# Performance work log

Hardware: AMD Instinct MI355X
Metric: run time of the kernel (lower is better)

Reference implementation:

```python
import jax, jax.numpy as jnp
import numpy as np

TRACE_LR = 0.1
TRACE_DECAY = 0.99
ERASE_LR = 1.0
EPS = 1e-8


def setup_inputs() -> dict:
    key = jax.random.key(0)
    k1, k2, k3, k4 = jax.random.split(key, 4)
    B, H, S, D = 8, 8, 4096, 64
    DM = 768
    Q = jax.random.normal(k1, (B, H, S, D), dtype=jnp.float32)
    V = jax.random.normal(k2, (B, H, S, D), dtype=jnp.float32)
    # value_traces buffer (small random state so erase path is non-trivial)
    trace = jax.random.normal(k3, (H, D, D), dtype=jnp.float32) * 0.01
    # W_out: Linear(H*D -> DM), weight shape (DM, H*D), out = x @ W.T
    W_out = jax.random.normal(k4, (DM, H * D), dtype=jnp.float32) / np.sqrt(H * D)
    return {"Q": Q, "V": V, "trace": trace, "W_out": W_out}


def _hebbian_write(Q, V, trace):
    """Erase-before-write + decayed Hebbian outer-product update.

    Q, V: (B, H, S, D); trace: (H, D, D). Shift-1 offset: key at i, value at i+2.
    """
    B, H, S, D = Q.shape
    Q_store = Q[:, :, :-2, :]            # (B,H,S-2,D)
    V_store = V[:, :, 2:, :]             # (B,H,S-2,D)
    denom = B * (S - 2)
    # reconsolidation erasure of old associations along normalized keys
    Q_norm = jnp.clip(jnp.linalg.norm(Q_store, axis=-1, keepdims=True), EPS)
    Q_erase = Q_store / Q_norm
    V_old = jnp.einsum('bhip,hpq->bhiq', Q_erase, trace)
    erase = jnp.einsum('bhip,bhiq->hpq', Q_erase, V_old) / denom
    trace = trace - ERASE_LR * erase
    # Hebbian outer-product write
    update = jnp.einsum('bhip,bhiq->hpq', Q_store, V_store) / denom
    return TRACE_DECAY * trace + TRACE_LR * update


def reference(Q, V, trace, W_out):
    B, H, S, D = Q.shape
    new_trace = _hebbian_write(Q, V, trace)
    # shift-1 retrieval: Q_addr at position i uses Q from position i-1
    Q_addr = jnp.concatenate(
        [jnp.zeros_like(Q[:, :, :1, :]), Q[:, :, :-1, :]], axis=2)  # (B,H,S,D)
    V_ret = jnp.einsum('bhsp,hpq->bhsq', Q_addr, new_trace)          # (B,H,S,D)
    V_ret = V_ret.transpose(0, 2, 1, 3).reshape(B, S, H * D)         # (B,S,H*D)
    return V_ret @ W_out.T                                           # (B,S,d_model)
```

## Files before the change

kernel.cpp:

```cpp
#include <hip/hip_runtime.h>

#define B_ 8
#define H_ 8
#define S_ 4096
#define D_ 64
#define DM_ 768
#define NSTORE 4094
#define DENOM 32752.0f

typedef short bfrag_t __attribute__((ext_vector_type(8)));
typedef float f32x4_t __attribute__((ext_vector_type(4)));
typedef unsigned short us8_t __attribute__((ext_vector_type(8)));

__device__ inline unsigned short f2bf(float x) {
    unsigned int u = __float_as_uint(x);
    unsigned int r = (u + 0x7fffu + ((u >> 16) & 1u)) >> 16;
    return (unsigned short)r;
}

__global__ __launch_bounds__(256, 2) void gram_kernel(
    const float* __restrict__ Q, const float* __restrict__ V,
    float* __restrict__ gG, float* __restrict__ gU,
    unsigned short* __restrict__ Qbf, int writeQbf) {
    const int split = blockIdx.x, h = blockIdx.y, b = blockIdx.z;
    const int t = threadIdx.x;
    const int wave = t >> 6, lane = t & 63;
    const int quad = lane >> 4, l15 = lane & 15;
    __shared__ float Qs[64][68];
    __shared__ float Vs[64][68];
    __shared__ float scale[64];
    __shared__ __align__(16) unsigned short QT[64][72];
    __shared__ __align__(16) unsigned short QnT[64][72];
    __shared__ __align__(16) unsigned short VT[64][72];

    const size_t bh = (size_t)(b * H_ + h);
    const float* Qbh = Q + bh * S_ * D_;
    const float* Vbh = V + bh * S_ * D_;
    unsigned short* Qbfbh = Qbf + bh * S_ * D_;

    f32x4_t accG[4] = {}, accU[4] = {};
    const int r0 = split * 512;

    for (int tile = 0; tile < 8; ++tile) {
        const int rbase = r0 + tile * 64;
        #pragma unroll
        for (int i = 0; i < 4; ++i) {
            int f = i * 256 + t;
            int row = f >> 4, c4 = f & 15;
            int r = rbase + row;
            float4 q4 = *(const float4*)(Qbh + (size_t)r * D_ + c4 * 4);
            if (writeQbf) {
                ushort4 u;
                u.x = f2bf(q4.x); u.y = f2bf(q4.y); u.z = f2bf(q4.z); u.w = f2bf(q4.w);
                *(ushort4*)(Qbfbh + (size_t)r * D_ + c4 * 4) = u;
            }
            float4 v4 = make_float4(0.f, 0.f, 0.f, 0.f);
            if (r < NSTORE) {
                v4 = *(const float4*)(Vbh + (size_t)(r + 2) * D_ + c4 * 4);
            } else {
                q4 = make_float4(0.f, 0.f, 0.f, 0.f);
            }
            *(float4*)(&Qs[row][c4 * 4]) = q4;
            *(float4*)(&Vs[row][c4 * 4]) = v4;
            float ss = q4.x * q4.x + q4.y * q4.y + q4.z * q4.z + q4.w * q4.w;
            ss += __shfl_xor(ss, 1);
            ss += __shfl_xor(ss, 2);
            ss += __shfl_xor(ss, 4);
            ss += __shfl_xor(ss, 8);
            if ((t & 15) == 0) scale[row] = 1.0f / fmaxf(ss, 1e-16f);
        }
        __syncthreads();
        #pragma unroll
        for (int it = 0; it < 2; ++it) {
            int idx = it * 256 + t;
            int p = idx & 63, oct = idx >> 6;
            us8_t qt, qn, vt;
            #pragma unroll
            for (int j = 0; j < 8; ++j) {
                int r = oct * 8 + j;
                float s = scale[r];
                float q = Qs[r][p];
                float v = Vs[r][p];
                qt[j] = f2bf(q);
                qn[j] = f2bf(q * s);
                vt[j] = f2bf(v);
            }
            *(us8_t*)(&QT[p][oct * 8])  = qt;
            *(us8_t*)(&QnT[p][oct * 8]) = qn;
            *(us8_t*)(&VT[p][oct * 8])  = vt;
        }
        __syncthreads();
        #pragma unroll
        for (int c = 0; c < 2; ++c) {
            int k0 = c * 32 + quad * 8;
            bfrag_t ag = *(const bfrag_t*)(&QnT[wave * 16 + l15][k0]);
            bfrag_t au = *(const bfrag_t*)(&QT[wave * 16 + l15][k0]);
            #pragma unroll
            for (int j = 0; j < 4; ++j) {
                bfrag_t bq = *(const bfrag_t*)(&QT[j * 16 + l15][k0]);
                bfrag_t bv = *(const bfrag_t*)(&VT[j * 16 + l15][k0]);
                accG[j] = __builtin_amdgcn_mfma_f32_16x16x32_bf16(ag, bq, accG[j], 0, 0, 0);
                accU[j] = __builtin_amdgcn_mfma_f32_16x16x32_bf16(au, bv, accU[j], 0, 0, 0);
            }
        }
        __syncthreads();
    }
    float* gGh = gG + h * 4096;
    float* gUh = gU + h * 4096;
    #pragma unroll
    for (int j = 0; j < 4; ++j) {
        int col = j * 16 + l15;
        #pragma unroll
        for (int r = 0; r < 4; ++r) {
            int row = wave * 16 + quad * 4 + r;
            atomicAdd(&gGh[row * 64 + col], accG[j][r]);
            atomicAdd(&gUh[row * 64 + col], accU[j][r]);
        }
    }
}

__global__ __launch_bounds__(256) void trace_kernel(
    const float* __restrict__ gG, const float* __restrict__ gU,
    const float* __restrict__ trace, float* __restrict__ Tnew) {
    const int h = blockIdx.x, t = threadIdx.x;
    __shared__ float Gs[64][64];
    __shared__ float Ts[64][64];
    const float* Gh = gG + h * 4096;
    const float* Uh = gU + h * 4096;
    const float* Th = trace + h * 4096;
    float* To = Tnew + h * 4096;
    for (int k = 0; k < 16; ++k) {
        int e = k * 256 + t;
        Gs[e >> 6][e & 63] = Gh[e];
        Ts[e >> 6][e & 63] = Th[e];
    }
    __syncthreads();
    const float inv_denom = 1.0f / DENOM;
    for (int k = 0; k < 16; ++k) {
        int e = k * 256 + t;
        int p = e >> 6, q = e & 63;
        float dot = 0.f;
        #pragma unroll
        for (int r = 0; r < 64; ++r) dot += Gs[p][r] * Ts[r][q];
        To[e] = 0.99f * (Ts[p][q] - dot * inv_denom) + 0.1f * (Uh[e] * inv_denom);
    }
}

__global__ __launch_bounds__(256) void wc_kernel(
    const float* __restrict__ Tnew, const float* __restrict__ Wout,
    unsigned short* __restrict__ WcT) {
    const int nc = blockIdx.x, h = blockIdx.y, t = threadIdx.x;
    __shared__ float TsT[64][64];
    __shared__ float Ws[4][64];
    const float* Th = Tnew + h * 4096;
    for (int k = 0; k < 16; ++k) {
        int e = k * 256 + t;
        TsT[e & 63][e >> 6] = Th[e];
    }
    __syncthreads();
    const int p = t & 63, sub = t >> 6;
    for (int i = 0; i < 32; ++i) {
        int n = nc * 128 + i * 4 + sub;
        Ws[sub][p] = Wout[(size_t)n * 512 + h * 64 + p];
        __syncthreads();
        float acc = 0.f;
        #pragma unroll
        for (int q = 0; q < 64; ++q) acc += TsT[q][p] * Ws[sub][q];
        WcT[(size_t)n * 512 + h * 64 + p] = f2bf(acc);
        __syncthreads();
    }
}

template <bool QBF>
__global__ __launch_bounds__(256, 2) void matmul_kernel(
    const float* __restrict__ Qf, const unsigned short* __restrict__ Qb,
    const unsigned short* __restrict__ WcT, float* __restrict__ out) {
    const int mTile = blockIdx.x;
    const int nTile = blockIdx.y;
    const int t = threadIdx.x;
    const int wave = t >> 6, lane = t & 63;
    const int wm = wave >> 1, wn = wave & 1;
    const int quad = lane >> 4, l15 = lane & 15;
    __shared__ __align__(16) unsigned short As[128][72];
    __shared__ __align__(16) unsigned short Bs[128][72];
    const int b = mTile >> 5;
    const int s0 = (mTile & 31) * 128;
    const int nBase = nTile * 128;
    f32x4_t acc[4][4] = {};

    for (int h = 0; h < 8; ++h) {
        const size_t bh = (size_t)(b * H_ + h);
        if (QBF) {
            const unsigned short* Qbh = Qb + bh * S_ * D_;
            #pragma unroll
            for (int i = 0; i < 4; ++i) {
                int f = i * 256 + t;
                int row = f >> 3, c8 = f & 7;
                int s = s0 + row;
                uint4 u = make_uint4(0, 0, 0, 0);
                if (s > 0) u = *(const uint4*)(Qbh + (size_t)(s - 1) * D_ + c8 * 8);
                *(uint4*)(&As[row][c8 * 8]) = u;
            }
        } else {
            const float* Qbh = Qf + bh * S_ * D_;
            #pragma unroll
            for (int i = 0; i < 8; ++i) {
                int f = i * 256 + t;
                int row = f >> 4, c4 = f & 15;
                int s = s0 + row;
                float4 q4 = make_float4(0.f, 0.f, 0.f, 0.f);
                if (s > 0) q4 = *(const float4*)(Qbh + (size_t)(s - 1) * D_ + c4 * 4);
                ushort4 u;
                u.x = f2bf(q4.x); u.y = f2bf(q4.y); u.z = f2bf(q4.z); u.w = f2bf(q4.w);
                *(ushort4*)(&As[row][c4 * 4]) = u;
            }
        }
        #pragma unroll
        for (int i = 0; i < 4; ++i) {
            int f = i * 256 + t;
            int row = f >> 3, c8 = f & 7;
            uint4 w = *(const uint4*)(WcT + (size_t)(nBase + row) * 512 + h * 64 + c8 * 8);
            *(uint4*)(&Bs[row][c8 * 8]) = w;
        }
        __syncthreads();
        #pragma unroll
        for (int c = 0; c < 2; ++c) {
            int k0 = c * 32 + quad * 8;
            bfrag_t af[4], bf[4];
            #pragma unroll
            for (int i = 0; i < 4; ++i)
                af[i] = *(const bfrag_t*)(&As[wm * 64 + i * 16 + l15][k0]);
            #pragma unroll
            for (int j = 0; j < 4; ++j)
                bf[j] = *(const bfrag_t*)(&Bs[wn * 64 + j * 16 + l15][k0]);
            #pragma unroll
            for (int i = 0; i < 4; ++i)
                #pragma unroll
                for (int j = 0; j < 4; ++j)
                    acc[i][j] = __builtin_amdgcn_mfma_f32_16x16x32_bf16(af[i], bf[j], acc[i][j], 0, 0, 0);
        }
        __syncthreads();
    }
    const size_t mBase = (size_t)mTile * 128;
    #pragma unroll
    for (int i = 0; i < 4; ++i) {
        int mrow = wm * 64 + i * 16 + quad * 4;
        #pragma unroll
        for (int j = 0; j < 4; ++j) {
            int n = nBase + wn * 64 + j * 16 + l15;
            #pragma unroll
            for (int r = 0; r < 4; ++r)
                out[(mBase + mrow + r) * DM_ + n] = acc[i][j][r];
        }
    }
}

extern "C" void kernel_launch(void* const* d_in, const int* in_sizes, int n_in,
                              void* d_out, int out_size, void* d_ws, size_t ws_size,
                              hipStream_t stream) {
    const float* Q     = (const float*)d_in[0];
    const float* V     = (const float*)d_in[1];
    const float* trace = (const float*)d_in[2];
    const float* Wout  = (const float*)d_in[3];
    float* out = (float*)d_out;

    float* gG   = (float*)d_ws;
    float* gU   = gG + 32768;
    float* Tnew = gU + 32768;
    unsigned short* WcT = (unsigned short*)(Tnew + 32768);
    unsigned short* Qbf = WcT + 393216;

    const size_t qbf_bytes = (size_t)B_ * H_ * S_ * D_ * 2;
    const size_t base_bytes = 3u * 32768u * 4u + 393216u * 2u;
    const int useQbf = (ws_size >= base_bytes + qbf_bytes) ? 1 : 0;

    hipMemsetAsync(d_ws, 0, 2 * 32768 * sizeof(float), stream);
    gram_kernel<<<dim3(8, 8, 8), 256, 0, stream>>>(Q, V, gG, gU, Qbf, useQbf);
    trace_kernel<<<8, 256, 0, stream>>>(gG, gU, trace, Tnew);
    wc_kernel<<<dim3(6, 8), 256, 0, stream>>>(Tnew, Wout, WcT);
    if (useQbf)
        matmul_kernel<true><<<dim3(256, 6), 256, 0, stream>>>(Q, Qbf, WcT, out);
    else
        matmul_kernel<false><<<dim3(256, 6), 256, 0, stream>>>(Q, Qbf, WcT, out);
}
```

Baseline: 306.3 us.

## Rework gram, trace, wc and matmul kernels with async LDS copies and partial-sum reduction

The gram kernel now transposes and converts directly into XOR-swizzled bf16 LDS tiles without fp32 staging. When workspace allows, it uses twice as many splits and writes per-slab partials that a separate reduce kernel sums, replacing atomics and the memset. The trace and wc kernels are register-tiled with vector LDS reads. The bf16 matmul uses global_load_lds async 16-byte copies into swizzled LDS with three blocks per CU. This trades extra workspace and a partial-sum buffer round trip for less LDS staging, fewer bank conflicts and no atomics.

```diff
diff --git a/kernel.cpp b/kernel.cpp
--- a/kernel.cpp
+++ b/kernel.cpp
@@ -10,7 +10,6 @@
 
 typedef short bfrag_t __attribute__((ext_vector_type(8)));
 typedef float f32x4_t __attribute__((ext_vector_type(4)));
-typedef unsigned short us8_t __attribute__((ext_vector_type(8)));
 
 __device__ inline unsigned short f2bf(float x) {
     unsigned int u = __float_as_uint(x);
@@ -18,113 +17,136 @@
     return (unsigned short)r;
 }
 
-__global__ __launch_bounds__(256, 2) void gram_kernel(
+__device__ inline void async_copy16(const void* g, void* lds) {
+    __builtin_amdgcn_global_load_lds((__attribute__((address_space(1))) void*)g,
+                                     (__attribute__((address_space(3))) void*)lds,
+                                     16, 0, 0);
+}
+
+#define MFMA16(a, b, c) __builtin_amdgcn_mfma_f32_16x16x32_bf16((a), (b), (c), 0, 0, 0)
+
+template <bool PART>
+__global__ __launch_bounds__(256, 4) void gram_kernel(
     const float* __restrict__ Q, const float* __restrict__ V,
     float* __restrict__ gG, float* __restrict__ gU,
-    unsigned short* __restrict__ Qbf, int writeQbf) {
+    unsigned short* __restrict__ Qbf, float* __restrict__ gP, int writeQbf) {
     const int split = blockIdx.x, h = blockIdx.y, b = blockIdx.z;
+    const int nsplit = gridDim.x;
+    const int rowsPer = 4096 / nsplit;
+    const int nTiles = rowsPer >> 6;
     const int t = threadIdx.x;
     const int wave = t >> 6, lane = t & 63;
     const int quad = lane >> 4, l15 = lane & 15;
-    __shared__ float Qs[64][68];
-    __shared__ float Vs[64][68];
-    __shared__ float scale[64];
-    __shared__ __align__(16) unsigned short QT[64][72];
-    __shared__ __align__(16) unsigned short QnT[64][72];
-    __shared__ __align__(16) unsigned short VT[64][72];
+    __shared__ __align__(16) unsigned short QT[64 * 64];
+    __shared__ __align__(16) unsigned short QnT[64 * 64];
+    __shared__ __align__(16) unsigned short VT[64 * 64];
 
     const size_t bh = (size_t)(b * H_ + h);
     const float* Qbh = Q + bh * S_ * D_;
     const float* Vbh = V + bh * S_ * D_;
-    unsigned short* Qbfbh = Qbf + bh * S_ * D_;
+    unsigned short* Qo = Qbf + bh * S_ * D_;
 
     f32x4_t accG[4] = {}, accU[4] = {};
-    const int r0 = split * 512;
-
-    for (int tile = 0; tile < 8; ++tile) {
+    const int r0 = split * rowsPer;
+
+    for (int tile = 0; tile < nTiles; ++tile) {
         const int rbase = r0 + tile * 64;
         #pragma unroll
         for (int i = 0; i < 4; ++i) {
             int f = i * 256 + t;
-            int row = f >> 4, c4 = f & 15;
-            int r = rbase + row;
+            int rowl = f >> 4, c4 = f & 15;
+            int r = rbase + rowl;
             float4 q4 = *(const float4*)(Qbh + (size_t)r * D_ + c4 * 4);
             if (writeQbf) {
                 ushort4 u;
                 u.x = f2bf(q4.x); u.y = f2bf(q4.y); u.z = f2bf(q4.z); u.w = f2bf(q4.w);
-                *(ushort4*)(Qbfbh + (size_t)r * D_ + c4 * 4) = u;
+                *(ushort4*)(Qo + (size_t)r * D_ + c4 * 4) = u;
             }
             float4 v4 = make_float4(0.f, 0.f, 0.f, 0.f);
-            if (r < NSTORE) {
-                v4 = *(const float4*)(Vbh + (size_t)(r + 2) * D_ + c4 * 4);
-            } else {
-                q4 = make_float4(0.f, 0.f, 0.f, 0.f);
-            }
-            *(float4*)(&Qs[row][c4 * 4]) = q4;
-            *(float4*)(&Vs[row][c4 * 4]) = v4;
+            if (r < NSTORE) v4 = *(const float4*)(Vbh + (size_t)(r + 2) * D_ + c4 * 4);
+            else q4 = make_float4(0.f, 0.f, 0.f, 0.f);
             float ss = q4.x * q4.x + q4.y * q4.y + q4.z * q4.z + q4.w * q4.w;
             ss += __shfl_xor(ss, 1);
             ss += __shfl_xor(ss, 2);
             ss += __shfl_xor(ss, 4);
             ss += __shfl_xor(ss, 8);
-            if ((t & 15) == 0) scale[row] = 1.0f / fmaxf(ss, 1e-16f);
-        }
-        __syncthreads();
-        #pragma unroll
-        for (int it = 0; it < 2; ++it) {
-            int idx = it * 256 + t;
-            int p = idx & 63, oct = idx >> 6;
-            us8_t qt, qn, vt;
-            #pragma unroll
-            for (int j = 0; j < 8; ++j) {
-                int r = oct * 8 + j;
-                float s = scale[r];
-                float q = Qs[r][p];
-                float v = Vs[r][p];
-                qt[j] = f2bf(q);
-                qn[j] = f2bf(q * s);
-                vt[j] = f2bf(v);
-            }
-            *(us8_t*)(&QT[p][oct * 8])  = qt;
-            *(us8_t*)(&QnT[p][oct * 8]) = qn;
-            *(us8_t*)(&VT[p][oct * 8])  = vt;
+            float sc = 1.0f / fmaxf(ss, 1e-16f);
+            int col = rowl ^ ((c4 & 7) << 3);
+            float qa[4] = {q4.x, q4.y, q4.z, q4.w};
+            float va[4] = {v4.x, v4.y, v4.z, v4.w};
+            #pragma unroll
+            for (int j = 0; j < 4; ++j) {
+                int p = c4 * 4 + j;
+                QT [p * 64 + col] = f2bf(qa[j]);
+                QnT[p * 64 + col] = f2bf(qa[j] * sc);
+                VT [p * 64 + col] = f2bf(va[j]);
+            }
         }
         __syncthreads();
         #pragma unroll
         for (int c = 0; c < 2; ++c) {
-            int k0 = c * 32 + quad * 8;
-            bfrag_t ag = *(const bfrag_t*)(&QnT[wave * 16 + l15][k0]);
-            bfrag_t au = *(const bfrag_t*)(&QT[wave * 16 + l15][k0]);
+            int pA = wave * 16 + l15;
+            int offA = pA * 64 + (((c * 4 + quad) ^ ((pA >> 2) & 7)) << 3);
+            bfrag_t ag = *(const bfrag_t*)&QnT[offA];
+            bfrag_t au = *(const bfrag_t*)&QT[offA];
             #pragma unroll
             for (int j = 0; j < 4; ++j) {
-                bfrag_t bq = *(const bfrag_t*)(&QT[j * 16 + l15][k0]);
-                bfrag_t bv = *(const bfrag_t*)(&VT[j * 16 + l15][k0]);
-                accG[j] = __builtin_amdgcn_mfma_f32_16x16x32_bf16(ag, bq, accG[j], 0, 0, 0);
-                accU[j] = __builtin_amdgcn_mfma_f32_16x16x32_bf16(au, bv, accU[j], 0, 0, 0);
-            }
-        }
-        __syncthreads();
-    }
-    float* gGh = gG + h * 4096;
-    float* gUh = gU + h * 4096;
-    #pragma unroll
-    for (int j = 0; j < 4; ++j) {
-        int col = j * 16 + l15;
-        #pragma unroll
-        for (int r = 0; r < 4; ++r) {
-            int row = wave * 16 + quad * 4 + r;
-            atomicAdd(&gGh[row * 64 + col], accG[j][r]);
-            atomicAdd(&gUh[row * 64 + col], accU[j][r]);
-        }
-    }
+                int pB = j * 16 + l15;
+                int offB = pB * 64 + (((c * 4 + quad) ^ ((pB >> 2) & 7)) << 3);
+                bfrag_t bq = *(const bfrag_t*)&QT[offB];
+                bfrag_t bv = *(const bfrag_t*)&VT[offB];
+                accG[j] = MFMA16(ag, bq, accG[j]);
+                accU[j] = MFMA16(au, bv, accU[j]);
+            }
+        }
+        __syncthreads();
+    }
+    if (PART) {
+        const int slab = split * 8 + b;
+        float* base = gP + ((size_t)(h * 128 + slab) * 2) * 4096;
+        #pragma unroll
+        for (int j = 0; j < 4; ++j) {
+            int coln = j * 16 + l15;
+            #pragma unroll
+            for (int r = 0; r < 4; ++r) {
+                int row = wave * 16 + quad * 4 + r;
+                base[row * 64 + coln]        = accG[j][r];
+                base[4096 + row * 64 + coln] = accU[j][r];
+            }
+        }
+    } else {
+        float* gGh = gG + h * 4096;
+        float* gUh = gU + h * 4096;
+        #pragma unroll
+        for (int j = 0; j < 4; ++j) {
+            int coln = j * 16 + l15;
+            #pragma unroll
+            for (int r = 0; r < 4; ++r) {
+                int row = wave * 16 + quad * 4 + r;
+                atomicAdd(&gGh[row * 64 + coln], accG[j][r]);
+                atomicAdd(&gUh[row * 64 + coln], accU[j][r]);
+            }
+        }
+    }
+}
+
+__global__ __launch_bounds__(256) void reduce_kernel(
+    const float* __restrict__ gP, float* __restrict__ gG, float* __restrict__ gU) {
+    const int h = blockIdx.x, chunk = blockIdx.y, t = threadIdx.x;
+    const int arr = t >> 7, idx = chunk * 128 + (t & 127);
+    const float* base = gP + ((size_t)(h * 128) * 2 + arr) * 4096 + idx;
+    float s = 0.f;
+    #pragma unroll 8
+    for (int sl = 0; sl < 128; ++sl) s += base[(size_t)sl * 2 * 4096];
+    (arr ? gU : gG)[h * 4096 + idx] = s;
 }
 
 __global__ __launch_bounds__(256) void trace_kernel(
     const float* __restrict__ gG, const float* __restrict__ gU,
     const float* __restrict__ trace, float* __restrict__ Tnew) {
     const int h = blockIdx.x, t = threadIdx.x;
-    __shared__ float Gs[64][64];
-    __shared__ float Ts[64][64];
+    __shared__ float Gs[64][68];
+    __shared__ float Ts[64][68];
     const float* Gh = gG + h * 4096;
     const float* Uh = gU + h * 4096;
     const float* Th = trace + h * 4096;
@@ -135,14 +157,24 @@
         Ts[e >> 6][e & 63] = Th[e];
     }
     __syncthreads();
-    const float inv_denom = 1.0f / DENOM;
-    for (int k = 0; k < 16; ++k) {
-        int e = k * 256 + t;
-        int p = e >> 6, q = e & 63;
-        float dot = 0.f;
-        #pragma unroll
-        for (int r = 0; r < 64; ++r) dot += Gs[p][r] * Ts[r][q];
-        To[e] = 0.99f * (Ts[p][q] - dot * inv_denom) + 0.1f * (Uh[e] * inv_denom);
+    const int p = t >> 2, q0 = (t & 3) * 16;
+    f32x4_t acc[4] = {};
+    for (int r = 0; r < 64; ++r) {
+        float g = Gs[p][r];
+        #pragma unroll
+        for (int i = 0; i < 4; ++i) {
+            f32x4_t tv = *(const f32x4_t*)&Ts[r][q0 + i * 4];
+            acc[i] += g * tv;
+        }
+    }
+    const float inv = 1.0f / DENOM;
+    #pragma unroll
+    for (int i = 0; i < 4; ++i) {
+        int e = p * 64 + q0 + i * 4;
+        f32x4_t ts = *(const f32x4_t*)&Ts[p][q0 + i * 4];
+        f32x4_t uu = *(const f32x4_t*)(Uh + e);
+        f32x4_t res = 0.99f * (ts - acc[i] * inv) + (0.1f * inv) * uu;
+        *(f32x4_t*)(To + e) = res;
     }
 }
 
@@ -150,33 +182,122 @@
     const float* __restrict__ Tnew, const float* __restrict__ Wout,
     unsigned short* __restrict__ WcT) {
     const int nc = blockIdx.x, h = blockIdx.y, t = threadIdx.x;
-    __shared__ float TsT[64][64];
-    __shared__ float Ws[4][64];
+    __shared__ float TsT[64][68];
+    __shared__ float WbT[64][132];
     const float* Th = Tnew + h * 4096;
-    for (int k = 0; k < 16; ++k) {
-        int e = k * 256 + t;
-        TsT[e & 63][e >> 6] = Th[e];
+    #pragma unroll
+    for (int i = 0; i < 4; ++i) {
+        int f = i * 256 + t;
+        int p = f >> 4, q4 = f & 15;
+        float4 v = *(const float4*)(Th + p * 64 + q4 * 4);
+        TsT[q4 * 4 + 0][p] = v.x; TsT[q4 * 4 + 1][p] = v.y;
+        TsT[q4 * 4 + 2][p] = v.z; TsT[q4 * 4 + 3][p] = v.w;
+    }
+    #pragma unroll
+    for (int i = 0; i < 8; ++i) {
+        int f = i * 256 + t;
+        int n = f >> 4, q4 = f & 15;
+        float4 w = *(const float4*)(Wout + (size_t)(nc * 128 + n) * 512 + h * 64 + q4 * 4);
+        WbT[q4 * 4 + 0][n] = w.x; WbT[q4 * 4 + 1][n] = w.y;
+        WbT[q4 * 4 + 2][n] = w.z; WbT[q4 * 4 + 3][n] = w.w;
     }
     __syncthreads();
-    const int p = t & 63, sub = t >> 6;
-    for (int i = 0; i < 32; ++i) {
-        int n = nc * 128 + i * 4 + sub;
-        Ws[sub][p] = Wout[(size_t)n * 512 + h * 64 + p];
-        __syncthreads();
-        float acc = 0.f;
-        #pragma unroll
-        for (int q = 0; q < 64; ++q) acc += TsT[q][p] * Ws[sub][q];
-        WcT[(size_t)n * 512 + h * 64 + p] = f2bf(acc);
-        __syncthreads();
-    }
-}
-
-template <bool QBF>
-__global__ __launch_bounds__(256, 2) void matmul_kernel(
-    const float* __restrict__ Qf, const unsigned short* __restrict__ Qb,
-    const unsigned short* __restrict__ WcT, float* __restrict__ out) {
+    const int n0 = (t >> 4) * 8, p0 = (t & 15) * 4;
+    f32x4_t acc[8] = {};
+    for (int q = 0; q < 64; ++q) {
+        f32x4_t tp = *(const f32x4_t*)&TsT[q][p0];
+        f32x4_t w0 = *(const f32x4_t*)&WbT[q][n0];
+        f32x4_t w1 = *(const f32x4_t*)&WbT[q][n0 + 4];
+        #pragma unroll
+        for (int i = 0; i < 4; ++i) acc[i] += w0[i] * tp;
+        #pragma unroll
+        for (int i = 0; i < 4; ++i) acc[4 + i] += w1[i] * tp;
+    }
+    #pragma unroll
+    for (int i = 0; i < 8; ++i) {
+        int n = nc * 128 + n0 + i;
+        ushort4 u;
+        u.x = f2bf(acc[i][0]); u.y = f2bf(acc[i][1]);
+        u.z = f2bf(acc[i][2]); u.w = f2bf(acc[i][3]);
+        *(ushort4*)(WcT + (size_t)n * 512 + h * 64 + p0) = u;
+    }
+}
+
+__global__ __launch_bounds__(256, 3) void matmul_fast(
+    const unsigned short* __restrict__ Qb, const unsigned short* __restrict__ WcT,
+    float* __restrict__ out) {
     const int mTile = blockIdx.x;
     const int nTile = blockIdx.y;
+    const int t = threadIdx.x;
+    const int wave = t >> 6, lane = t & 63;
+    const int wm = wave >> 1, wn = wave & 1;
+    const int quad = lane >> 4, l15 = lane & 15;
+    __shared__ __align__(16) unsigned short As[128 * 64];
+    __shared__ __align__(16) unsigned short Bs[128 * 64];
+    const int b = mTile >> 5;
+    const int s0 = (mTile & 31) * 128;
+    const int nBase = nTile * 128;
+    const int rl8 = lane >> 3, g = lane & 7;
+    const int gs = g ^ rl8;
+    f32x4_t acc[4][4] = {};
+
+    for (int h = 0; h < 8; ++h) {
+        const unsigned short* Qbh = Qb + (size_t)(b * H_ + h) * S_ * D_;
+        #pragma unroll
+        for (int k = 0; k < 4; ++k) {
+            int ch = wave * 4 + k;
+            int row = ch * 8 + rl8;
+            int s = s0 + row;
+            int sc = (s > 0) ? (s - 1) : 0;
+            async_copy16(Qbh + (size_t)sc * 64 + gs * 8, &As[ch * 512 + lane * 8]);
+            async_copy16(WcT + (size_t)(nBase + row) * 512 + h * 64 + gs * 8,
+                         &Bs[ch * 512 + lane * 8]);
+        }
+        __syncthreads();
+        if (s0 == 0) {
+            if (t < 8) ((uint4*)As)[t] = make_uint4(0, 0, 0, 0);
+            __syncthreads();
+        }
+        #pragma unroll
+        for (int c = 0; c < 2; ++c) {
+            int gk = c * 4 + quad;
+            bfrag_t af[4], bf[4];
+            #pragma unroll
+            for (int i = 0; i < 4; ++i) {
+                int row = wm * 64 + i * 16 + l15;
+                af[i] = *(const bfrag_t*)&As[row * 64 + ((gk ^ (row & 7)) << 3)];
+            }
+            #pragma unroll
+            for (int j = 0; j < 4; ++j) {
+                int row = wn * 64 + j * 16 + l15;
+                bf[j] = *(const bfrag_t*)&Bs[row * 64 + ((gk ^ (row & 7)) << 3)];
+            }
+            #pragma unroll
+            for (int i = 0; i < 4; ++i)
+                #pragma unroll
+                for (int j = 0; j < 4; ++j)
+                    acc[i][j] = MFMA16(af[i], bf[j], acc[i][j]);
+        }
+        __syncthreads();
+    }
+    const size_t mBase = (size_t)mTile * 128;
+    #pragma unroll
+    for (int i = 0; i < 4; ++i) {
+        int mrow = wm * 64 + i * 16 + quad * 4;
+        #pragma unroll
+        for (int j = 0; j < 4; ++j) {
+            int n = nBase + wn * 64 + j * 16 + l15;
+            #pragma unroll
+            for (int r = 0; r < 4; ++r)
+                out[(mBase + mrow + r) * DM_ + n] = acc[i][j][r];
+        }
+    }
+}
+
+__global__ __launch_bounds__(256, 2) void matmul_f32(
+    const float* __restrict__ Qf, const unsigned short* __restrict__ WcT,
+    float* __restrict__ out) {
+    const int mTile = blockIdx.x, nTile = blockIdx.y;
     const int t = threadIdx.x;
     const int wave = t >> 6, lane = t & 63;
     const int wm = wave >> 1, wn = wave & 1;
@@ -187,33 +308,18 @@
     const int s0 = (mTile & 31) * 128;
     const int nBase = nTile * 128;
     f32x4_t acc[4][4] = {};
-
     for (int h = 0; h < 8; ++h) {
-        const size_t bh = (size_t)(b * H_ + h);
-        if (QBF) {
-            const unsigned short* Qbh = Qb + bh * S_ * D_;
-            #pragma unroll
-            for (int i = 0; i < 4; ++i) {
-                int f = i * 256 + t;
-                int row = f >> 3, c8 = f & 7;
-                int s = s0 + row;
-                uint4 u = make_uint4(0, 0, 0, 0);
-                if (s > 0) u = *(const uint4*)(Qbh + (size_t)(s - 1) * D_ + c8 * 8);
-                *(uint4*)(&As[row][c8 * 8]) = u;
-            }
-        } else {
-            const float* Qbh = Qf + bh * S_ * D_;
-            #pragma unroll
-            for (int i = 0; i < 8; ++i) {
-                int f = i * 256 + t;
-                int row = f >> 4, c4 = f & 15;
-                int s = s0 + row;
-                float4 q4 = make_float4(0.f, 0.f, 0.f, 0.f);
-                if (s > 0) q4 = *(const float4*)(Qbh + (size_t)(s - 1) * D_ + c4 * 4);
-                ushort4 u;
-                u.x = f2bf(q4.x); u.y = f2bf(q4.y); u.z = f2bf(q4.z); u.w = f2bf(q4.w);
-                *(ushort4*)(&As[row][c4 * 4]) = u;
-            }
+        const float* Qbh = Qf + (size_t)(b * H_ + h) * S_ * D_;
+        #pragma unroll
+        for (int i = 0; i < 8; ++i) {
+            int f = i * 256 + t;
+            int row = f >> 4, c4 = f & 15;
+            int s = s0 + row;
+            float4 q4 = make_float4(0.f, 0.f, 0.f, 0.f);
+            if (s > 0) q4 = *(const float4*)(Qbh + (size_t)(s - 1) * D_ + c4 * 4);
+            ushort4 u;
+            u.x = f2bf(q4.x); u.y = f2bf(q4.y); u.z = f2bf(q4.z); u.w = f2bf(q4.w);
+            *(ushort4*)(&As[row][c4 * 4]) = u;
         }
         #pragma unroll
         for (int i = 0; i < 4; ++i) {
@@ -237,7 +343,7 @@
             for (int i = 0; i < 4; ++i)
                 #pragma unroll
                 for (int j = 0; j < 4; ++j)
-                    acc[i][j] = __builtin_amdgcn_mfma_f32_16x16x32_bf16(af[i], bf[j], acc[i][j], 0, 0, 0);
+                    acc[i][j] = MFMA16(af[i], bf[j], acc[i][j]);
         }
         __syncthreads();
     }
@@ -269,17 +375,23 @@
     float* Tnew = gU + 32768;
     unsigned short* WcT = (unsigned short*)(Tnew + 32768);
     unsigned short* Qbf = WcT + 393216;
-
-    const size_t qbf_bytes = (size_t)B_ * H_ * S_ * D_ * 2;
-    const size_t base_bytes = 3u * 32768u * 4u + 393216u * 2u;
-    const int useQbf = (ws_size >= base_bytes + qbf_bytes) ? 1 : 0;
-
-    hipMemsetAsync(d_ws, 0, 2 * 32768 * sizeof(float), stream);
-    gram_kernel<<<dim3(8, 8, 8), 256, 0, stream>>>(Q, V, gG, gU, Qbf, useQbf);
+    float* gP = (float*)(Qbf + (size_t)B_ * H_ * S_ * D_);
+
+    const size_t needQbf  = 1179648u + 33554432u;
+    const size_t needFull = needQbf + 33554432u;
+    const int mode = (ws_size >= needFull) ? 2 : ((ws_size >= needQbf) ? 1 : 0);
+
+    if (mode == 2) {
+        gram_kernel<true><<<dim3(16, 8, 8), 256, 0, stream>>>(Q, V, gG, gU, Qbf, gP, 1);
+        reduce_kernel<<<dim3(8, 32), 256, 0, stream>>>(gP, gG, gU);
+    } else {
+        hipMemsetAsync(d_ws, 0, 2 * 32768 * sizeof(float), stream);
+        gram_kernel<false><<<dim3(8, 8, 8), 256, 0, stream>>>(Q, V, gG, gU, Qbf, gP, mode >= 1);
+    }
     trace_kernel<<<8, 256, 0, stream>>>(gG, gU, trace, Tnew);
     wc_kernel<<<dim3(6, 8), 256, 0, stream>>>(Tnew, Wout, WcT);
-    if (useQbf)
-        matmul_kernel<true><<<dim3(256, 6), 256, 0, stream>>>(Q, Qbf, WcT, out);
+    if (mode >= 1)
+        matmul_fast<<<dim3(256, 6), 256, 0, stream>>>(Qbf, WcT, out);
     else
-        matmul_kernel<false><<<dim3(256, 6), 256, 0, stream>>>(Q, Qbf, WcT, out);
-}
+        matmul_f32<<<dim3(256, 6), 256, 0, stream>>>(Q, WcT, out);
+}
```

New measurement: 266.6 us. 13.0% less time.
